# Kernel optimization log

Hardware: AMD Instinct MI355X
Metric: run time of the kernel (lower is better)

Reference implementation:

```python
import jax, jax.numpy as jnp
import numpy as np

B, H1, H2, D, C = 4096, 32, 32, 32, 64


def setup_inputs() -> dict:
    key = jax.random.key(0)
    k1, k2, k3 = jax.random.split(key, 3)
    x = jax.random.normal(k1, (B, H1, D), dtype=jnp.float32)
    y = jax.random.normal(k2, (B, H2, D), dtype=jnp.float32)
    # glorot-uniform-ish kernel of shape (compress_dim, H1, H2)
    limit = float(np.sqrt(6.0 / (H1 + H2)))
    kernel = jax.random.uniform(k3, (C, H1, H2), dtype=jnp.float32,
                                minval=-limit, maxval=limit)
    return {"x": x, "y": y, "kernel": kernel}


def reference(x, y, kernel):
    # Original math: outer[b,i,j,d] = x[b,i,d]*y[b,j,d];
    # output_mat[b,c,d] = sum_{i,j} outer[b,i,j,d] * kernel[c,i,j]
    # Expressed as a fused bilinear contraction (avoids the [B,H1,H2,D] tensor):
    # first fold kernel into y per compress channel, then contract with x.
    t = jnp.einsum('cij,bjd->bcid', kernel, y)       # [B,C,H1,D]
    output_mat = jnp.einsum('bid,bcid->bcd', x, t)   # [B,C,D]
    final_output = jnp.sum(output_mat, axis=-1)      # [B,C]
    return (output_mat, final_output)
```

## Files before the change

kernel.cpp:

```cpp
#include <hip/hip_runtime.h>
#include <hip/hip_fp16.h>


typedef __attribute__((ext_vector_type(8))) _Float16 half8;
typedef __attribute__((ext_vector_type(2))) __fp16 fp16x2;
typedef __attribute__((ext_vector_type(4))) float f32x4;
typedef __attribute__((ext_vector_type(8))) short short8;

__device__ __forceinline__ unsigned int dup_h(float f) {
    union { fp16x2 h; unsigned int u; } w;
    w.h = __builtin_amdgcn_cvt_pkrtz(f, f);
    return w.u;
}
__device__ __forceinline__ fp16x2 pk2(float a, float b) {
    return __builtin_amdgcn_cvt_pkrtz(a, b);
}

__global__ __launch_bounds__(256) void kswz_kernel(const float* __restrict__ kern,
                                                   unsigned short* __restrict__ kswz) {
    int idx  = blockIdx.x * 256 + threadIdx.x;
    int lane = idx & 63;
    int nt   = (idx >> 6) & 3;
    int s    = idx >> 8;
    int c    = nt * 16 + (lane & 15);
    int jb   = (lane >> 4) * 8;
    const float* src = kern + c * 1024 + s * 32 + jb;
    union { half8 h; short8 s8; } v;
#pragma unroll
    for (int t = 0; t < 8; ++t) v.h[t] = (_Float16)src[t];
    *(short8*)(kswz + (size_t)idx * 8) = v.s8;
}

__device__ __forceinline__ void gld_lds16(const void* g, void* l) {
    __builtin_amdgcn_global_load_lds(
        (const __attribute__((address_space(1))) unsigned int*)g,
        (__attribute__((address_space(3))) unsigned int*)l, 16, 0, 0);
}

__global__ __launch_bounds__(256, 2) void cin_main(const float* __restrict__ x,
                                                   const float* __restrict__ y,
                                                   const unsigned short* __restrict__ kswz,
                                                   float* __restrict__ out_mat,
                                                   float* __restrict__ out_fin) {
    __shared__ unsigned int xs[8 * 1024];
    __shared__ __align__(16) unsigned short kb[2][8192];

    const int tid  = threadIdx.x;
    const int wave = tid >> 6;
    const int lane = tid & 63;
    const int quad = lane >> 4;
    const int n16  = lane & 15;
    const int b_blk = blockIdx.x * 8;
    const int cq0   = blockIdx.x & 7;

#pragma unroll
    for (int r = 0; r < 4; ++r)
        gld_lds16(kswz + (size_t)cq0 * 8192 + (r * 256 + tid) * 8,
                  &kb[0][r * 2048 + wave * 512]);

    {
        const float4* xg4 = (const float4*)(x + (size_t)b_blk * 1024);
#pragma unroll
        for (int r = 0; r < 8; ++r) {
            int i4 = r * 256 + tid;
            float4 v = xg4[i4];
            uint4 w;
            w.x = dup_h(v.x); w.y = dup_h(v.y); w.z = dup_h(v.z); w.w = dup_h(v.w);
            *(uint4*)&xs[i4 * 4] = w;
        }
    }

    const int bpair = wave;
    const int b0 = b_blk + bpair * 2;
    fp16x2 yv2[4][4];
#pragma unroll
    for (int mt = 0; mt < 4; ++mt) {
        const int b = b0 + (mt >> 1);
        const int d = n16 + 16 * (mt & 1);
        const float* yp = y + (size_t)b * 1024 + (quad * 8) * 32 + d;
#pragma unroll
        for (int p = 0; p < 4; ++p)
            yv2[mt][p] = pk2(yp[(2 * p) * 32], yp[(2 * p + 1) * 32]);
    }

    f32x4 acc[4][4];
#pragma unroll
    for (int mt = 0; mt < 4; ++mt)
#pragma unroll
        for (int nt = 0; nt < 4; ++nt) acc[mt][nt] = (f32x4){0.f, 0.f, 0.f, 0.f};

    int xoff[4];
#pragma unroll
    for (int mt = 0; mt < 4; ++mt)
        xoff[mt] = (bpair * 2 + (mt >> 1)) * 1024 + n16 + 16 * (mt & 1);

    __syncthreads();

    for (int p8 = 0; p8 < 8; ++p8) {
        if (p8 < 7) {
            const int cn = (cq0 + p8 + 1) & 7;
            unsigned short* dst = &kb[(p8 + 1) & 1][0];
#pragma unroll
            for (int r = 0; r < 4; ++r)
                gld_lds16(kswz + (size_t)cn * 8192 + (r * 256 + tid) * 8,
                          dst + r * 2048 + wave * 512);
        }

        const unsigned short* kbase = &kb[p8 & 1][0];
        const int sb = ((cq0 + p8) & 7) * 4;
#pragma unroll
        for (int k = 0; k < 4; ++k) {
            half8 bf[4];
#pragma unroll
            for (int nt = 0; nt < 4; ++nt)
                bf[nt] = *(const half8*)(kbase + ((k * 4 + nt) * 64 + lane) * 8);
#pragma unroll
            for (int mt = 0; mt < 4; ++mt) {
                union { unsigned int u; fp16x2 h; } xv;
                xv.u = xs[xoff[mt] + (sb + k) * 32];
                union { half8 h8; fp16x2 h2[4]; } af;
#pragma unroll
                for (int p = 0; p < 4; ++p) af.h2[p] = xv.h * yv2[mt][p];
#pragma unroll
                for (int nt = 0; nt < 4; ++nt)
                    acc[mt][nt] = __builtin_amdgcn_mfma_f32_16x16x32_f16(
                        af.h8, bf[nt], acc[mt][nt], 0, 0, 0);
            }
        }
        __syncthreads();
    }

#pragma unroll
    for (int mt = 0; mt < 4; ++mt) {
        const int b = b0 + (mt >> 1);
        const int dbase = 16 * (mt & 1) + quad * 4;
#pragma unroll
        for (int nt = 0; nt < 4; ++nt) {
            const int c = nt * 16 + n16;
            *(f32x4*)(out_mat + (size_t)b * 2048 + c * 32 + dbase) = acc[mt][nt];
        }
    }

#pragma unroll
    for (int a = 0; a < 2; ++a) {
        const int b = b0 + a;
#pragma unroll
        for (int nt = 0; nt < 4; ++nt) {
            float f = 0.f;
#pragma unroll
            for (int t = 0; t < 4; ++t) f += acc[2 * a][nt][t] + acc[2 * a + 1][nt][t];
            f += __shfl_xor(f, 16);
            f += __shfl_xor(f, 32);
            if (lane < 16) out_fin[(size_t)b * 64 + nt * 16 + n16] = f;
        }
    }
}

extern "C" void kernel_launch(void* const* d_in, const int* in_sizes, int n_in,
                              void* d_out, int out_size, void* d_ws, size_t ws_size,
                              hipStream_t stream) {
    const float* x    = (const float*)d_in[0];
    const float* y    = (const float*)d_in[1];
    const float* kern = (const float*)d_in[2];
    float* out_mat = (float*)d_out;
    float* out_fin = (float*)d_out + 4096 * 64 * 32;
    unsigned short* kswz = (unsigned short*)d_ws;

    kswz_kernel<<<32, 256, 0, stream>>>(kern, kswz);
    cin_main<<<512, 256, 0, stream>>>(x, y, kswz, out_mat, out_fin);
}
```

Before: 100.8 us.

## Split K across wave pairs, read kernel from global, halve batch per block

Each block now handles 4 batch rows instead of 8. The 32-step i-reduction is split between two wave halves, which combine their partial accumulators through shared memory before writing. The double-buffered LDS staging of the swizzled kernel is dropped: B fragments are read straight from global/L2, with a per-block rotation of the start step to spread accesses. The goal is a smaller LDS footprint so more blocks fit per CU, and a doubled grid to raise occupancy, at the cost of extra global kernel reads and an LDS reduction step.

```diff
diff --git a/kernel.cpp b/kernel.cpp
--- a/kernel.cpp
+++ b/kernel.cpp
@@ -31,37 +31,29 @@
     *(short8*)(kswz + (size_t)idx * 8) = v.s8;
 }
 
-__device__ __forceinline__ void gld_lds16(const void* g, void* l) {
-    __builtin_amdgcn_global_load_lds(
-        (const __attribute__((address_space(1))) unsigned int*)g,
-        (__attribute__((address_space(3))) unsigned int*)l, 16, 0, 0);
-}
-
-__global__ __launch_bounds__(256, 2) void cin_main(const float* __restrict__ x,
+__global__ __launch_bounds__(256, 4) void cin_main(const float* __restrict__ x,
                                                    const float* __restrict__ y,
                                                    const unsigned short* __restrict__ kswz,
                                                    float* __restrict__ out_mat,
                                                    float* __restrict__ out_fin) {
-    __shared__ unsigned int xs[8 * 1024];
-    __shared__ __align__(16) unsigned short kb[2][8192];
+    __shared__ __align__(16) unsigned char smem[32768];
+    unsigned int* xs = (unsigned int*)smem;
+    f32x4* red = (f32x4*)smem;
 
     const int tid  = threadIdx.x;
     const int wave = tid >> 6;
     const int lane = tid & 63;
     const int quad = lane >> 4;
     const int n16  = lane & 15;
-    const int b_blk = blockIdx.x * 8;
-    const int cq0   = blockIdx.x & 7;
-
-#pragma unroll
-    for (int r = 0; r < 4; ++r)
-        gld_lds16(kswz + (size_t)cq0 * 8192 + (r * 256 + tid) * 8,
-                  &kb[0][r * 2048 + wave * 512]);
+    const int bpair = wave & 1;
+    const int khalf = wave >> 1;
+    const int b_blk = blockIdx.x * 4;
+    const int b0 = b_blk + bpair * 2;
 
     {
         const float4* xg4 = (const float4*)(x + (size_t)b_blk * 1024);
 #pragma unroll
-        for (int r = 0; r < 8; ++r) {
+        for (int r = 0; r < 4; ++r) {
             int i4 = r * 256 + tid;
             float4 v = xg4[i4];
             uint4 w;
@@ -70,8 +62,6 @@
         }
     }
 
-    const int bpair = wave;
-    const int b0 = b_blk + bpair * 2;
     fp16x2 yv2[4][4];
 #pragma unroll
     for (int mt = 0; mt < 4; ++mt) {
@@ -94,64 +84,73 @@
     for (int mt = 0; mt < 4; ++mt)
         xoff[mt] = (bpair * 2 + (mt >> 1)) * 1024 + n16 + 16 * (mt & 1);
 
+    const char* kl = (const char*)kswz + lane * 16;
+    const int rot = blockIdx.x & 15;
+
     __syncthreads();
 
-    for (int p8 = 0; p8 < 8; ++p8) {
-        if (p8 < 7) {
-            const int cn = (cq0 + p8 + 1) & 7;
-            unsigned short* dst = &kb[(p8 + 1) & 1][0];
 #pragma unroll
-            for (int r = 0; r < 4; ++r)
-                gld_lds16(kswz + (size_t)cn * 8192 + (r * 256 + tid) * 8,
-                          dst + r * 2048 + wave * 512);
-        }
-
-        const unsigned short* kbase = &kb[p8 & 1][0];
-        const int sb = ((cq0 + p8) & 7) * 4;
+    for (int k = 0; k < 16; ++k) {
+        const int s = khalf * 16 + ((k + rot) & 15);
+        half8 bf[4];
 #pragma unroll
-        for (int k = 0; k < 4; ++k) {
-            half8 bf[4];
+        for (int nt = 0; nt < 4; ++nt)
+            bf[nt] = *(const half8*)(kl + s * 4096 + nt * 1024);
+#pragma unroll
+        for (int mt = 0; mt < 4; ++mt) {
+            union { unsigned int u; fp16x2 h; } xv;
+            xv.u = xs[xoff[mt] + s * 32];
+            union { half8 h8; fp16x2 h2[4]; } af;
+#pragma unroll
+            for (int p = 0; p < 4; ++p) af.h2[p] = xv.h * yv2[mt][p];
 #pragma unroll
             for (int nt = 0; nt < 4; ++nt)
-                bf[nt] = *(const half8*)(kbase + ((k * 4 + nt) * 64 + lane) * 8);
-#pragma unroll
-            for (int mt = 0; mt < 4; ++mt) {
-                union { unsigned int u; fp16x2 h; } xv;
-                xv.u = xs[xoff[mt] + (sb + k) * 32];
-                union { half8 h8; fp16x2 h2[4]; } af;
-#pragma unroll
-                for (int p = 0; p < 4; ++p) af.h2[p] = xv.h * yv2[mt][p];
-#pragma unroll
-                for (int nt = 0; nt < 4; ++nt)
-                    acc[mt][nt] = __builtin_amdgcn_mfma_f32_16x16x32_f16(
-                        af.h8, bf[nt], acc[mt][nt], 0, 0, 0);
-            }
-        }
-        __syncthreads();
-    }
-
-#pragma unroll
-    for (int mt = 0; mt < 4; ++mt) {
-        const int b = b0 + (mt >> 1);
-        const int dbase = 16 * (mt & 1) + quad * 4;
-#pragma unroll
-        for (int nt = 0; nt < 4; ++nt) {
-            const int c = nt * 16 + n16;
-            *(f32x4*)(out_mat + (size_t)b * 2048 + c * 32 + dbase) = acc[mt][nt];
+                acc[mt][nt] = __builtin_amdgcn_mfma_f32_16x16x32_f16(
+                    af.h8, bf[nt], acc[mt][nt], 0, 0, 0);
         }
     }
 
+    __syncthreads();
+    if (khalf == 1) {
 #pragma unroll
-    for (int a = 0; a < 2; ++a) {
-        const int b = b0 + a;
+        for (int mt = 0; mt < 4; ++mt)
 #pragma unroll
-        for (int nt = 0; nt < 4; ++nt) {
-            float f = 0.f;
+            for (int nt = 0; nt < 4; ++nt)
+                red[(bpair * 16 + mt * 4 + nt) * 64 + lane] = acc[mt][nt];
+    }
+    __syncthreads();
+    if (khalf == 0) {
 #pragma unroll
-            for (int t = 0; t < 4; ++t) f += acc[2 * a][nt][t] + acc[2 * a + 1][nt][t];
-            f += __shfl_xor(f, 16);
-            f += __shfl_xor(f, 32);
-            if (lane < 16) out_fin[(size_t)b * 64 + nt * 16 + n16] = f;
+        for (int mt = 0; mt < 4; ++mt)
+#pragma unroll
+            for (int nt = 0; nt < 4; ++nt) {
+                f32x4 o = red[(bpair * 16 + mt * 4 + nt) * 64 + lane];
+                acc[mt][nt] += o;
+            }
+
+#pragma unroll
+        for (int mt = 0; mt < 4; ++mt) {
+            const int b = b0 + (mt >> 1);
+            const int dbase = 16 * (mt & 1) + quad * 4;
+#pragma unroll
+            for (int nt = 0; nt < 4; ++nt) {
+                const int c = nt * 16 + n16;
+                *(f32x4*)(out_mat + (size_t)b * 2048 + c * 32 + dbase) = acc[mt][nt];
+            }
+        }
+
+#pragma unroll
+        for (int a = 0; a < 2; ++a) {
+            const int b = b0 + a;
+#pragma unroll
+            for (int nt = 0; nt < 4; ++nt) {
+                float f = 0.f;
+#pragma unroll
+                for (int t = 0; t < 4; ++t) f += acc[2 * a][nt][t] + acc[2 * a + 1][nt][t];
+                f += __shfl_xor(f, 16);
+                f += __shfl_xor(f, 32);
+                if (lane < 16) out_fin[(size_t)b * 64 + nt * 16 + n16] = f;
+            }
         }
     }
 }
@@ -167,5 +166,5 @@
     unsigned short* kswz = (unsigned short*)d_ws;
 
     kswz_kernel<<<32, 256, 0, stream>>>(kern, kswz);
-    cin_main<<<512, 256, 0, stream>>>(x, y, kswz, out_mat, out_fin);
+    cin_main<<<1024, 256, 0, stream>>>(x, y, kswz, out_mat, out_fin);
 }
```

Measured after the change: 103.4 us. +2.6%, slower.
